# Performance work log

Measured on AMD Instinct MI355X. Metric: run time of the kernel, lower is better.

The kernel has to match this reference:

```python
import jax, jax.numpy as jnp
import numpy as np

H = 1024; NH = 16; HD = H // NH  # hidden, heads, head_dim

def setup_inputs() -> dict:
    key = jax.random.key(0)
    ks = jax.random.split(key, 9)
    s = 1.0 / np.sqrt(H)
    return {
        "hidden_states": jax.random.normal(ks[0], (2, 2048, H), jnp.float32),
        "Wq": jax.random.uniform(ks[1], (H, H), jnp.float32, -s, s),
        "bq": jnp.zeros((H,), jnp.float32),
        "Wk": jax.random.uniform(ks[2], (H, H), jnp.float32, -s, s),
        "bk": jnp.zeros((H,), jnp.float32),
        "Wv": jax.random.uniform(ks[3], (H, H), jnp.float32, -s, s),
        "bv": jnp.zeros((H,), jnp.float32),
        "Wo": jax.random.uniform(ks[4], (H, H), jnp.float32, -s, s),
        "bo": jnp.zeros((H,), jnp.float32),
    }

def reference(hidden_states, Wq, bq, Wk, bk, Wv, bv, Wo, bo):
    B, S, _ = hidden_states.shape
    def heads(x):  # [B,S,H] -> [B,NH,S,HD]
        return x.reshape(B, S, NH, HD).transpose(0, 2, 1, 3)
    q = heads(hidden_states @ Wq + bq)
    k = heads(hidden_states @ Wk + bk)
    v = heads(hidden_states @ Wv + bv)
    scores = jnp.einsum('bhqd,bhkd->bhqk', q, k) / jnp.sqrt(jnp.float32(HD))
    causal = jnp.where(jnp.tril(jnp.ones((S, S), bool)), 0.0, -jnp.inf)
    probs = jax.nn.softmax(scores + causal[None, None], axis=-1)
    ctx = jnp.einsum('bhqk,bhkd->bhqd', probs, v)
    ctx = ctx.transpose(0, 2, 1, 3).reshape(B, S, H)
    return ctx @ Wo + bo
```

## Files before the change

### kernel.cpp

```cpp
#include <hip/hip_runtime.h>
#include <hip/hip_bf16.h>

#define BB 2
#define SS 2048
#define HH 1024
#define NHH 16
#define HDD 64
#define MM (BB*SS)
#define QKV_N (3*HH)

typedef _Float16 f16x8 __attribute__((ext_vector_type(8)));
typedef _Float16 f16x4 __attribute__((ext_vector_type(4)));
typedef float f32x4 __attribute__((ext_vector_type(4)));

#define MFMA16(a,b,c)  __builtin_amdgcn_mfma_f32_16x16x32_f16((a),(b),(c),0,0,0)
#define MFMA16K16(a,b,c) __builtin_amdgcn_mfma_f32_16x16x16f16((a),(b),(c),0,0,0)

__device__ __forceinline__ void gl2lds16(const _Float16* g, _Float16* l) {
    __builtin_amdgcn_global_load_lds(
        (const __attribute__((address_space(1))) void*)g,
        (__attribute__((address_space(3))) void*)l, 16, 0, 0);
}

__device__ __forceinline__ float fexp2(float x) { return __builtin_amdgcn_exp2f(x); }

__global__ __launch_bounds__(256) void prep_kernel(
    const float* __restrict__ X,
    const float* __restrict__ W0, const float* __restrict__ W1,
    const float* __restrict__ W2, const float* __restrict__ W3,
    _Float16* __restrict__ Xh,
    _Float16* __restrict__ WqkvT, _Float16* __restrict__ WoT)
{
    __shared__ float t[64][65];
    int z = blockIdx.z;
    int tid = threadIdx.x;
    if (z == 4) {
        int base = (blockIdx.y * 16 + blockIdx.x) * 256 + tid;
        const float4* xin = (const float4*)X;
        f16x4* xout = (f16x4*)Xh;
#pragma unroll
        for (int i = 0; i < 16; ++i) {
            float4 v = xin[base + i * 65536];
            f16x4 hh = {(_Float16)v.x, (_Float16)v.y, (_Float16)v.z, (_Float16)v.w};
            xout[base + i * 65536] = hh;
        }
        return;
    }
    const float* src = (z == 0) ? W0 : (z == 1) ? W1 : (z == 2) ? W2 : W3;
    _Float16* dst = (z < 3) ? (WqkvT + (size_t)z * HH * HH) : WoT;
    int k0 = blockIdx.y * 64, n0 = blockIdx.x * 64;
#pragma unroll
    for (int p = 0; p < 4; ++p) {
        int row = p * 16 + (tid >> 4);
        int col4 = (tid & 15) * 4;
        float4 v = *(const float4*)&src[(size_t)(k0 + row) * HH + n0 + col4];
        t[row][col4 + 0] = v.x; t[row][col4 + 1] = v.y;
        t[row][col4 + 2] = v.z; t[row][col4 + 3] = v.w;
    }
    __syncthreads();
#pragma unroll
    for (int p = 0; p < 2; ++p) {
        int nc = p * 32 + (tid >> 3);
        int ch = tid & 7;
        f16x8 o;
#pragma unroll
        for (int j = 0; j < 8; ++j) o[j] = (_Float16)t[ch * 8 + j][nc];
        *(f16x8*)&dst[(size_t)(n0 + nc) * HH + k0 + ch * 8] = o;
    }
}

template<int MODE>
__global__ __launch_bounds__(256) void gemm128_kernel(
    const _Float16* __restrict__ A, const _Float16* __restrict__ Bt,
    const float* __restrict__ bias0, const float* __restrict__ bias1, const float* __restrict__ bias2,
    _Float16* __restrict__ Qh, _Float16* __restrict__ Kh, _Float16* __restrict__ Vt,
    float* __restrict__ Out)
{
    const int K = HH;
    const int NT = K / 32;
    __shared__ _Float16 smem[24576];

    int row0 = blockIdx.y * 128, n0 = blockIdx.x * 128;
    int tid = threadIdx.x;
    int w = tid >> 6, l = tid & 63, m16 = l & 15, quad = l >> 4;
    int wm = w >> 1, wn = w & 1;

    int srow = w * 32 + (l >> 2);
    int sch = (l & 3) ^ ((l >> 2) & 3) ^ ((l >> 4) & 3);
    const _Float16* aptr = A + (size_t)(row0 + srow) * K + sch * 8;
    const _Float16* bptr = Bt + (size_t)(n0 + srow) * K + sch * 8;

    int gsw = (m16 & 3) ^ ((m16 >> 2) & 3);
    int acol = (quad ^ gsw) * 8;

    f32x4 zero4 = {0.f, 0.f, 0.f, 0.f};
    f32x4 acc[4][4];
#pragma unroll
    for (int i = 0; i < 4; ++i)
#pragma unroll
        for (int j = 0; j < 4; ++j) acc[i][j] = zero4;

    auto stage = [&](int t, int s) {
        int k0 = t * 32;
        int ao = s * 4096 + (w * 32) * 32;
        int bo = 12288 + s * 4096 + (w * 32) * 32;
        gl2lds16(aptr + k0, smem + ao);
        gl2lds16(aptr + (size_t)16 * K + k0, smem + ao + 16 * 32);
        gl2lds16(bptr + k0, smem + bo);
        gl2lds16(bptr + (size_t)16 * K + k0, smem + bo + 16 * 32);
    };

    stage(0, 0);
    stage(1, 1);
    int cur = 0;
    for (int t = 0; t < NT; ++t) {
        if (t < NT - 1) asm volatile("s_waitcnt vmcnt(4)" ::: "memory");
        else            asm volatile("s_waitcnt vmcnt(0)" ::: "memory");
        asm volatile("s_barrier" ::: "memory");
        if (t + 2 < NT) {
            int nxt = cur + 2; if (nxt >= 3) nxt -= 3;
            stage(t + 2, nxt);
        }
        const _Float16* Asr = smem + cur * 4096;
        const _Float16* Bsr = smem + 12288 + cur * 4096;
        f16x8 af[4], bf[4];
#pragma unroll
        for (int i = 0; i < 4; ++i)
            af[i] = *(const f16x8*)&Asr[(wm * 64 + i * 16 + m16) * 32 + acol];
#pragma unroll
        for (int j = 0; j < 4; ++j)
            bf[j] = *(const f16x8*)&Bsr[(wn * 64 + j * 16 + m16) * 32 + acol];
#pragma unroll
        for (int i = 0; i < 4; ++i)
#pragma unroll
            for (int j = 0; j < 4; ++j)
                acc[i][j] = MFMA16(af[i], bf[j], acc[i][j]);
        cur = (cur == 2) ? 0 : cur + 1;
    }

    if (MODE == 1) {
#pragma unroll
        for (int j = 0; j < 4; ++j) {
            int n = n0 + wn * 64 + j * 16 + m16;
            float bi = bias0[n];
#pragma unroll
            for (int i = 0; i < 4; ++i)
#pragma unroll
                for (int r = 0; r < 4; ++r) {
                    int mg = row0 + wm * 64 + i * 16 + quad * 4 + r;
                    Out[(size_t)mg * HH + n] = acc[i][j][r] + bi;
                }
        }
        return;
    }

    int which = n0 >> 10;
    const float* bias = (which == 0) ? bias0 : (which == 1) ? bias1 : bias2;
    __syncthreads();
#pragma unroll
    for (int j = 0; j < 4; ++j) {
        int n_local = wn * 64 + j * 16 + m16;
        float bi = bias[(n0 + n_local) & 1023];
#pragma unroll
        for (int i = 0; i < 4; ++i)
#pragma unroll
            for (int r = 0; r < 4; ++r) {
                int m_local = wm * 64 + i * 16 + quad * 4 + r;
                float v = acc[i][j][r] + bi;
                if (which == 0) v *= 0.18033688011112042f;
                if (which == 2) smem[n_local * 132 + m_local] = (_Float16)v;
                else            smem[m_local * 132 + n_local] = (_Float16)v;
            }
    }
    __syncthreads();

    int b = row0 >> 11, s0 = row0 & 2047;
    if (which == 2) {
#pragma unroll
        for (int p = 0; p < 8; ++p) {
            int n_local = p * 16 + (tid >> 4);
            int schunk = tid & 15;
            f16x8 v = *(const f16x8*)&smem[n_local * 132 + schunk * 8];
            int nw = (n0 + n_local) & 1023;
            int hh = nw >> 6, d = nw & 63;
            *(f16x8*)&Vt[((size_t)(b * NHH + hh) * HDD + d) * SS + s0 + schunk * 8] = v;
        }
    } else {
        _Float16* dst = (which == 0) ? Qh : Kh;
        int hh0 = (n0 & 1023) >> 6;
#pragma unroll
        for (int p = 0; p < 8; ++p) {
            int m_local = p * 16 + (tid >> 4);
            int seg = tid & 15;
            f16x8 v = *(const f16x8*)&smem[m_local * 132 + seg * 8];
            int hh = hh0 + (seg >> 3), d = (seg & 7) * 8;
            *(f16x8*)&dst[((size_t)(b * NHH + hh) * SS + s0 + m_local) * HDD + d] = v;
        }
    }
}

__global__ __launch_bounds__(512, 4) void attn_kernel(
    const _Float16* __restrict__ Qh, const _Float16* __restrict__ Kh,
    const _Float16* __restrict__ Vt, _Float16* __restrict__ Ctx)
{
    __shared__ _Float16 KV[3 * 8192];

    int tid = threadIdx.x;
    int w = tid >> 6, l = tid & 63;
    int m16 = l & 15, quad = l >> 4;
    int b = blockIdx.z, h = blockIdx.y;
    int tA = blockIdx.x, tB = 31 - tA;
    int half = w >> 2, wq = w & 3;
    int myT = half ? tB : tA;

    const _Float16* Q = Qh + (size_t)(b * NHH + h) * SS * HDD;
    const _Float16* K = Kh + (size_t)(b * NHH + h) * SS * HDD;
    const _Float16* V = Vt + (size_t)(b * NHH + h) * HDD * SS;

    int q = myT * 64 + wq * 16 + m16;
    f16x8 aq0 = *(const f16x8*)(Q + (size_t)q * HDD + quad * 8);
    f16x8 aq1 = *(const f16x8*)(Q + (size_t)q * HDD + 32 + quad * 8);

    int srow = w * 8 + (l >> 3);
    int sch = (l & 7) ^ (l >> 3);
    const _Float16* kg = K + (size_t)srow * HDD + sch * 8;
    const _Float16* vg = V + (size_t)srow * SS + sch * 8;

    auto stage = [&](int t, int s) {
        int kt = t * 64;
        _Float16* kb = &KV[s * 8192];
        _Float16* vb = &KV[s * 8192 + 4096];
        gl2lds16(kg + (size_t)kt * HDD, kb + (w * 8) * 64);
        gl2lds16(vg + kt, vb + (w * 8) * 64);
    };

    int swz = m16 & 7;
    int cka = (quad ^ swz) * 8;
    int ckb = ((quad + 4) ^ swz) * 8;
    int vco[4];
#pragma unroll
    for (int s = 0; s < 4; ++s)
        vco[s] = (((s * 2 + (quad >> 1)) ^ swz) * 8) + (quad & 1) * 4;

    f32x4 zero4 = {0.f, 0.f, 0.f, 0.f};
    const f16x4 ones4 = {(_Float16)1.f, (_Float16)1.f, (_Float16)1.f, (_Float16)1.f};
    f32x4 o[4];
#pragma unroll
    for (int c = 0; c < 4; ++c) o[c] = zero4;
    f32x4 lacc = zero4;

    stage(0, 0);
    stage(1, 1);
    int cur = 0;
    for (int t = 0; t <= tB; ++t) {
        int kt = t * 64;
        if (t < tB) asm volatile("s_waitcnt vmcnt(2)" ::: "memory");
        else        asm volatile("s_waitcnt vmcnt(0)" ::: "memory");
        asm volatile("s_barrier" ::: "memory");
        if (t + 2 <= tB) {
            int nxt = cur + 2; if (nxt >= 3) nxt -= 3;
            stage(t + 2, nxt);
        }

        if (t <= myT) {
            const _Float16* kb = &KV[cur * 8192];
            const _Float16* vb = &KV[cur * 8192 + 4096];
            f16x8 bk[4][2];
#pragma unroll
            for (int s = 0; s < 4; ++s) {
                const _Float16* kr = kb + (s * 16 + m16) * 64;
                bk[s][0] = *(const f16x8*)(kr + cka);
                bk[s][1] = *(const f16x8*)(kr + ckb);
            }
            f16x4 av[4][4];
#pragma unroll
            for (int c = 0; c < 4; ++c) {
                const _Float16* vr = vb + (c * 16 + m16) * 64;
#pragma unroll
                for (int s = 0; s < 4; ++s)
                    av[c][s] = *(const f16x4*)(vr + vco[s]);
            }

            f32x4 st[4];
#pragma unroll
            for (int s = 0; s < 4; ++s) {
                st[s] = MFMA16(bk[s][0], aq0, zero4);
                st[s] = MFMA16(bk[s][1], aq1, st[s]);
            }
            f16x4 pt[4];
            if (t == myT) {
#pragma unroll
                for (int s = 0; s < 4; ++s)
#pragma unroll
                    for (int r = 0; r < 4; ++r) {
                        float p = fexp2(st[s][r]);
                        int key = kt + s * 16 + quad * 4 + r;
                        if (key > q) p = 0.f;
                        pt[s][r] = (_Float16)p;
                    }
            } else {
#pragma unroll
                for (int s = 0; s < 4; ++s)
#pragma unroll
                    for (int r = 0; r < 4; ++r)
                        pt[s][r] = (_Float16)fexp2(st[s][r]);
            }
#pragma unroll
            for (int s = 0; s < 4; ++s)
                lacc = MFMA16K16(ones4, pt[s], lacc);
#pragma unroll
            for (int c = 0; c < 4; ++c)
#pragma unroll
                for (int s = 0; s < 4; ++s)
                    o[c] = MFMA16K16(av[c][s], pt[s], o[c]);
        }

        cur = (cur == 2) ? 0 : cur + 1;
    }

    float inv = 1.0f / lacc[0];
    size_t rowoff = ((size_t)(b * SS) + q) * HH + h * HDD;
#pragma unroll
    for (int c = 0; c < 4; ++c) {
        f16x4 ov;
#pragma unroll
        for (int r = 0; r < 4; ++r) ov[r] = (_Float16)(o[c][r] * inv);
        *(f16x4*)&Ctx[rowoff + c * 16 + quad * 4] = ov;
    }
}

extern "C" void kernel_launch(void* const* d_in, const int* in_sizes, int n_in,
                              void* d_out, int out_size, void* d_ws, size_t ws_size,
                              hipStream_t stream) {
    const float* hs = (const float*)d_in[0];
    const float* Wq = (const float*)d_in[1];
    const float* bq = (const float*)d_in[2];
    const float* Wk = (const float*)d_in[3];
    const float* bk = (const float*)d_in[4];
    const float* Wv = (const float*)d_in[5];
    const float* bv = (const float*)d_in[6];
    const float* Wo = (const float*)d_in[7];
    const float* bo = (const float*)d_in[8];
    float* out = (float*)d_out;

    size_t off = 0;
    auto alloc = [&](size_t bytes) {
        void* p = (char*)d_ws + off;
        off += (bytes + 255) & ~(size_t)255;
        return p;
    };
    _Float16* Xh    = (_Float16*)alloc((size_t)MM * HH * 2);
    _Float16* WqkvT = (_Float16*)alloc((size_t)3 * HH * HH * 2);
    _Float16* WoT   = (_Float16*)alloc((size_t)HH * HH * 2);
    _Float16* Qh    = (_Float16*)alloc((size_t)BB * NHH * SS * HDD * 2);
    _Float16* Kh    = (_Float16*)alloc((size_t)BB * NHH * SS * HDD * 2);
    _Float16* Vt    = (_Float16*)alloc((size_t)BB * NHH * SS * HDD * 2);
    _Float16* Ctx   = (_Float16*)alloc((size_t)MM * HH * 2);

    prep_kernel<<<dim3(16, 16, 5), 256, 0, stream>>>(
        hs, Wq, Wk, Wv, Wo, Xh, WqkvT, WoT);
    gemm128_kernel<0><<<dim3(QKV_N / 128, MM / 128), 256, 0, stream>>>(
        Xh, WqkvT, bq, bk, bv, Qh, Kh, Vt, nullptr);
    attn_kernel<<<dim3(16, NHH, BB), 512, 0, stream>>>(Qh, Kh, Vt, Ctx);
    gemm128_kernel<1><<<dim3(HH / 128, MM / 128), 256, 0, stream>>>(
        Ctx, WoT, bo, bo, bo, nullptr, nullptr, nullptr, out);
}
```

Before: 181.2 us.

## Use 256x256-tile 8-wave GEMM with XCD-aware block swizzle for QKV projection

Adds a new QKV projection GEMM that uses 256x256 output tiles with 512 threads and double-buffered direct global-to-LDS loads. Prefetch of the next K-slice is interleaved with the MFMA groups, and s_setprio raises priority around the MFMAs. Workgroup IDs are remapped in a swizzle across groups of 8, apparently to match the MI355X's XCDs and improve L2 reuse. The aim is more data reuse per loaded tile and fewer global reads, at the cost of a smaller grid (192 blocks), heavier register pressure, and an epilogue split into four passes through LDS.

```diff
diff --git a/kernel.cpp b/kernel.cpp
--- a/kernel.cpp
+++ b/kernel.cpp
@@ -69,6 +69,149 @@
     }
 }
 
+__global__ __launch_bounds__(512, 2) void gemm256_kernel(
+    const _Float16* __restrict__ A, const _Float16* __restrict__ Bt,
+    const float* __restrict__ bias0, const float* __restrict__ bias1, const float* __restrict__ bias2,
+    _Float16* __restrict__ Qh, _Float16* __restrict__ Kh, _Float16* __restrict__ Vt)
+{
+    const int K = HH;
+    const int NT = K / 32;
+    __shared__ _Float16 smem[32768];
+
+    int nwgx = gridDim.x;
+    int bid = blockIdx.y * nwgx + blockIdx.x;
+    int nwg = nwgx * gridDim.y;
+    int swzb = (bid & 7) * (nwg >> 3) + (bid >> 3);
+    int bx = swzb % nwgx, by = swzb / nwgx;
+    int row0 = by * 256, n0 = bx * 256;
+
+    int tid = threadIdx.x;
+    int w = tid >> 6, l = tid & 63, m16 = l & 15, quad = l >> 4;
+    int wm = w >> 2, wn = w & 3;
+
+    int sch = (l & 3) ^ ((l >> 2) & 3) ^ ((l >> 4) & 3);
+    const _Float16* aptr = A + (size_t)(row0 + w * 16 + (l >> 2)) * K + sch * 8;
+    const _Float16* bptr = Bt + (size_t)(n0 + w * 16 + (l >> 2)) * K + sch * 8;
+
+    int gsw = (m16 & 3) ^ ((m16 >> 2) & 3);
+    int acol = (quad ^ gsw) * 8;
+
+    f32x4 zero4 = {0.f, 0.f, 0.f, 0.f};
+    f32x4 acc[8][4];
+#pragma unroll
+    for (int i = 0; i < 8; ++i)
+#pragma unroll
+        for (int j = 0; j < 4; ++j) acc[i][j] = zero4;
+
+    auto stageA = [&](int t, int j) {
+        int s = (t & 1) * 16384;
+        gl2lds16(aptr + (size_t)j * 128 * K + t * 32, smem + s + (j * 128 + w * 16) * 32);
+    };
+    auto stageB = [&](int t, int j) {
+        int s = (t & 1) * 16384;
+        gl2lds16(bptr + (size_t)j * 128 * K + t * 32, smem + s + 8192 + (j * 128 + w * 16) * 32);
+    };
+
+    stageA(0, 0); stageA(0, 1); stageB(0, 0); stageB(0, 1);
+
+    for (int t = 0; t < NT; ++t) {
+        const _Float16* As = smem + (t & 1) * 16384;
+        const _Float16* Bs = As + 8192;
+        bool pf = (t + 1 < NT);
+
+        if (pf) { stageA(t + 1, 0); asm volatile("s_waitcnt vmcnt(1)" ::: "memory"); }
+        else    {                   asm volatile("s_waitcnt vmcnt(0)" ::: "memory"); }
+        asm volatile("s_barrier" ::: "memory");
+        f16x8 bf[4];
+#pragma unroll
+        for (int j = 0; j < 4; ++j)
+            bf[j] = *(const f16x8*)&Bs[(wn * 64 + j * 16 + m16) * 32 + acol];
+        {
+            f16x8 a0 = *(const f16x8*)&As[(wm * 128 + m16) * 32 + acol];
+            f16x8 a1 = *(const f16x8*)&As[(wm * 128 + 16 + m16) * 32 + acol];
+            __builtin_amdgcn_s_setprio(1);
+#pragma unroll
+            for (int j = 0; j < 4; ++j) acc[0][j] = MFMA16(a0, bf[j], acc[0][j]);
+#pragma unroll
+            for (int j = 0; j < 4; ++j) acc[1][j] = MFMA16(a1, bf[j], acc[1][j]);
+            __builtin_amdgcn_s_setprio(0);
+        }
+
+#pragma unroll
+        for (int p = 1; p < 4; ++p) {
+            f16x8 a0 = *(const f16x8*)&As[(wm * 128 + (2 * p) * 16 + m16) * 32 + acol];
+            f16x8 a1 = *(const f16x8*)&As[(wm * 128 + (2 * p + 1) * 16 + m16) * 32 + acol];
+            if (pf) {
+                if (p == 1) stageA(t + 1, 1);
+                else if (p == 2) stageB(t + 1, 0);
+                else stageB(t + 1, 1);
+            }
+            asm volatile("s_barrier" ::: "memory");
+            __builtin_amdgcn_s_setprio(1);
+#pragma unroll
+            for (int j = 0; j < 4; ++j) acc[2 * p][j] = MFMA16(a0, bf[j], acc[2 * p][j]);
+#pragma unroll
+            for (int j = 0; j < 4; ++j) acc[2 * p + 1][j] = MFMA16(a1, bf[j], acc[2 * p + 1][j]);
+            __builtin_amdgcn_s_setprio(0);
+        }
+        asm volatile("s_barrier" ::: "memory");
+    }
+
+    int which = n0 >> 10;
+    const float* bias = (which == 0) ? bias0 : (which == 1) ? bias1 : bias2;
+    int b = row0 >> 11, s0 = row0 & 2047;
+    _Float16* es = smem;
+
+#pragma unroll
+    for (int rh = 0; rh < 2; ++rh)
+#pragma unroll
+    for (int ch = 0; ch < 2; ++ch) {
+        __syncthreads();
+        if (wm == rh && (wn >> 1) == ch) {
+#pragma unroll
+            for (int j = 0; j < 4; ++j) {
+                int n_local = (wn & 1) * 64 + j * 16 + m16;
+                float bi = bias[(n0 + ch * 128 + n_local) & 1023];
+#pragma unroll
+                for (int i = 0; i < 8; ++i)
+#pragma unroll
+                    for (int r = 0; r < 4; ++r) {
+                        int m_local = i * 16 + quad * 4 + r;
+                        float v = acc[i][j][r] + bi;
+                        if (which == 0) v *= 0.18033688011112042f;
+                        if (which == 2) es[n_local * 132 + m_local] = (_Float16)v;
+                        else            es[m_local * 132 + n_local] = (_Float16)v;
+                    }
+            }
+        }
+        __syncthreads();
+        int hn0 = n0 + ch * 128;
+        int hs0 = s0 + rh * 128;
+        if (which == 2) {
+#pragma unroll
+            for (int p = 0; p < 4; ++p) {
+                int n_local = p * 32 + (tid >> 4);
+                int schunk = tid & 15;
+                f16x8 v = *(const f16x8*)&es[n_local * 132 + schunk * 8];
+                int nw = (hn0 + n_local) & 1023;
+                int hh = nw >> 6, d = nw & 63;
+                *(f16x8*)&Vt[((size_t)(b * NHH + hh) * HDD + d) * SS + hs0 + schunk * 8] = v;
+            }
+        } else {
+            _Float16* dst = (which == 0) ? Qh : Kh;
+            int hh0 = (hn0 & 1023) >> 6;
+#pragma unroll
+            for (int p = 0; p < 4; ++p) {
+                int m_local = p * 32 + (tid >> 4);
+                int seg = tid & 15;
+                f16x8 v = *(const f16x8*)&es[m_local * 132 + seg * 8];
+                int hh = hh0 + (seg >> 3), d = (seg & 7) * 8;
+                *(f16x8*)&dst[((size_t)(b * NHH + hh) * SS + hs0 + m_local) * HDD + d] = v;
+            }
+        }
+    }
+}
+
 template<int MODE>
 __global__ __launch_bounds__(256) void gemm128_kernel(
     const _Float16* __restrict__ A, const _Float16* __restrict__ Bt,
@@ -359,8 +502,8 @@
 
     prep_kernel<<<dim3(16, 16, 5), 256, 0, stream>>>(
         hs, Wq, Wk, Wv, Wo, Xh, WqkvT, WoT);
-    gemm128_kernel<0><<<dim3(QKV_N / 128, MM / 128), 256, 0, stream>>>(
-        Xh, WqkvT, bq, bk, bv, Qh, Kh, Vt, nullptr);
+    gemm256_kernel<<<dim3(QKV_N / 256, MM / 256), 512, 0, stream>>>(
+        Xh, WqkvT, bq, bk, bv, Qh, Kh, Vt);
     attn_kernel<<<dim3(16, NHH, BB), 512, 0, stream>>>(Qh, Kh, Vt, Ctx);
     gemm128_kernel<1><<<dim3(HH / 128, MM / 128), 256, 0, stream>>>(
         Ctx, WoT, bo, bo, bo, nullptr, nullptr, nullptr, out);
```

Result: slower. 199.1 us (+9.8%).

## Split paired causal tiles into one 256-thread block per query tile

Applied to the files above, without the earlier changes.

The attention kernel previously paired query tile t with tile 31-t inside a 512-thread block so every block did balanced work, with a triple-buffered K/V pipeline two tiles deep. It now launches one 256-thread block per 64-row query tile, longest tiles first, and uses a double-buffered pipeline that prefetches one tile ahead, with two barriers per iteration. This drops idle half-block iterations and the shared K/V loads they wasted, and lowers LDS use per block to allow more resident blocks. In exchange it relies on the hardware scheduler for load balance across uneven causal tiles and has a shallower prefetch.

```diff
diff --git a/kernel.cpp b/kernel.cpp
--- a/kernel.cpp
+++ b/kernel.cpp
@@ -199,39 +199,39 @@
     }
 }
 
-__global__ __launch_bounds__(512, 4) void attn_kernel(
+__global__ __launch_bounds__(256, 5) void attn_kernel(
     const _Float16* __restrict__ Qh, const _Float16* __restrict__ Kh,
     const _Float16* __restrict__ Vt, _Float16* __restrict__ Ctx)
 {
-    __shared__ _Float16 KV[3 * 8192];
+    __shared__ _Float16 KV[2 * 8192];
 
     int tid = threadIdx.x;
     int w = tid >> 6, l = tid & 63;
     int m16 = l & 15, quad = l >> 4;
     int b = blockIdx.z, h = blockIdx.y;
-    int tA = blockIdx.x, tB = 31 - tA;
-    int half = w >> 2, wq = w & 3;
-    int myT = half ? tB : tA;
+    int tq = 31 - blockIdx.x;
 
     const _Float16* Q = Qh + (size_t)(b * NHH + h) * SS * HDD;
     const _Float16* K = Kh + (size_t)(b * NHH + h) * SS * HDD;
     const _Float16* V = Vt + (size_t)(b * NHH + h) * HDD * SS;
 
-    int q = myT * 64 + wq * 16 + m16;
+    int q = tq * 64 + w * 16 + m16;
     f16x8 aq0 = *(const f16x8*)(Q + (size_t)q * HDD + quad * 8);
     f16x8 aq1 = *(const f16x8*)(Q + (size_t)q * HDD + 32 + quad * 8);
 
-    int srow = w * 8 + (l >> 3);
+    int srow = w * 16 + (l >> 3);
     int sch = (l & 7) ^ (l >> 3);
     const _Float16* kg = K + (size_t)srow * HDD + sch * 8;
     const _Float16* vg = V + (size_t)srow * SS + sch * 8;
 
-    auto stage = [&](int t, int s) {
+    auto stage = [&](int t) {
         int kt = t * 64;
-        _Float16* kb = &KV[s * 8192];
-        _Float16* vb = &KV[s * 8192 + 4096];
-        gl2lds16(kg + (size_t)kt * HDD, kb + (w * 8) * 64);
-        gl2lds16(vg + kt, vb + (w * 8) * 64);
+        _Float16* kb = &KV[(t & 1) * 8192];
+        _Float16* vb = &KV[(t & 1) * 8192 + 4096];
+        gl2lds16(kg + (size_t)kt * HDD, kb + (w * 16) * 64);
+        gl2lds16(kg + (size_t)(kt + 8) * HDD, kb + (w * 16 + 8) * 64);
+        gl2lds16(vg + kt, vb + (w * 16) * 64);
+        gl2lds16(vg + (size_t)8 * SS + kt, vb + (w * 16 + 8) * 64);
     };
 
     int swz = m16 & 7;
@@ -249,73 +249,68 @@
     for (int c = 0; c < 4; ++c) o[c] = zero4;
     f32x4 lacc = zero4;
 
-    stage(0, 0);
-    stage(1, 1);
-    int cur = 0;
-    for (int t = 0; t <= tB; ++t) {
+    stage(0);
+    for (int t = 0; t <= tq; ++t) {
         int kt = t * 64;
-        if (t < tB) asm volatile("s_waitcnt vmcnt(2)" ::: "memory");
-        else        asm volatile("s_waitcnt vmcnt(0)" ::: "memory");
         asm volatile("s_barrier" ::: "memory");
-        if (t + 2 <= tB) {
-            int nxt = cur + 2; if (nxt >= 3) nxt -= 3;
-            stage(t + 2, nxt);
-        }
-
-        if (t <= myT) {
-            const _Float16* kb = &KV[cur * 8192];
-            const _Float16* vb = &KV[cur * 8192 + 4096];
-            f16x8 bk[4][2];
-#pragma unroll
-            for (int s = 0; s < 4; ++s) {
-                const _Float16* kr = kb + (s * 16 + m16) * 64;
-                bk[s][0] = *(const f16x8*)(kr + cka);
-                bk[s][1] = *(const f16x8*)(kr + ckb);
-            }
-            f16x4 av[4][4];
-#pragma unroll
-            for (int c = 0; c < 4; ++c) {
-                const _Float16* vr = vb + (c * 16 + m16) * 64;
-#pragma unroll
-                for (int s = 0; s < 4; ++s)
-                    av[c][s] = *(const f16x4*)(vr + vco[s]);
-            }
-
-            f32x4 st[4];
-#pragma unroll
-            for (int s = 0; s < 4; ++s) {
-                st[s] = MFMA16(bk[s][0], aq0, zero4);
-                st[s] = MFMA16(bk[s][1], aq1, st[s]);
-            }
-            f16x4 pt[4];
-            if (t == myT) {
-#pragma unroll
-                for (int s = 0; s < 4; ++s)
-#pragma unroll
-                    for (int r = 0; r < 4; ++r) {
-                        float p = fexp2(st[s][r]);
-                        int key = kt + s * 16 + quad * 4 + r;
-                        if (key > q) p = 0.f;
-                        pt[s][r] = (_Float16)p;
-                    }
-            } else {
-#pragma unroll
-                for (int s = 0; s < 4; ++s)
-#pragma unroll
-                    for (int r = 0; r < 4; ++r)
-                        pt[s][r] = (_Float16)fexp2(st[s][r]);
-            }
+        if (t + 1 <= tq) {
+            stage(t + 1);
+            asm volatile("s_waitcnt vmcnt(4)" ::: "memory");
+        } else {
+            asm volatile("s_waitcnt vmcnt(0)" ::: "memory");
+        }
+        asm volatile("s_barrier" ::: "memory");
+
+        const _Float16* kb = &KV[(t & 1) * 8192];
+        const _Float16* vb = &KV[(t & 1) * 8192 + 4096];
+        f16x8 bk[4][2];
+#pragma unroll
+        for (int s = 0; s < 4; ++s) {
+            const _Float16* kr = kb + (s * 16 + m16) * 64;
+            bk[s][0] = *(const f16x8*)(kr + cka);
+            bk[s][1] = *(const f16x8*)(kr + ckb);
+        }
+        f16x4 av[4][4];
+#pragma unroll
+        for (int c = 0; c < 4; ++c) {
+            const _Float16* vr = vb + (c * 16 + m16) * 64;
 #pragma unroll
             for (int s = 0; s < 4; ++s)
-                lacc = MFMA16K16(ones4, pt[s], lacc);
-#pragma unroll
-            for (int c = 0; c < 4; ++c)
-#pragma unroll
-                for (int s = 0; s < 4; ++s)
-                    o[c] = MFMA16K16(av[c][s], pt[s], o[c]);
-        }
-
-        cur = (cur == 2) ? 0 : cur + 1;
+                av[c][s] = *(const f16x4*)(vr + vco[s]);
+        }
+
+        f32x4 st[4];
+#pragma unroll
+        for (int s = 0; s < 4; ++s) {
+            st[s] = MFMA16(bk[s][0], aq0, zero4);
+            st[s] = MFMA16(bk[s][1], aq1, st[s]);
+        }
+        f16x4 pt[4];
+        if (t == tq) {
+#pragma unroll
+            for (int s = 0; s < 4; ++s)
+#pragma unroll
+                for (int r = 0; r < 4; ++r) {
+                    float p = fexp2(st[s][r]);
+                    int key = kt + s * 16 + quad * 4 + r;
+                    if (key > q) p = 0.f;
+                    pt[s][r] = (_Float16)p;
+                }
+        } else {
+#pragma unroll
+            for (int s = 0; s < 4; ++s)
+#pragma unroll
+                for (int r = 0; r < 4; ++r)
+                    pt[s][r] = (_Float16)fexp2(st[s][r]);
+        }
+#pragma unroll
+        for (int s = 0; s < 4; ++s)
+            lacc = MFMA16K16(ones4, pt[s], lacc);
+#pragma unroll
+        for (int c = 0; c < 4; ++c)
+#pragma unroll
+            for (int s = 0; s < 4; ++s)
+                o[c] = MFMA16K16(av[c][s], pt[s], o[c]);
     }
 
     float inv = 1.0f / lacc[0];
@@ -361,7 +356,7 @@
         hs, Wq, Wk, Wv, Wo, Xh, WqkvT, WoT);
     gemm128_kernel<0><<<dim3(QKV_N / 128, MM / 128), 256, 0, stream>>>(
         Xh, WqkvT, bq, bk, bv, Qh, Kh, Vt, nullptr);
-    attn_kernel<<<dim3(16, NHH, BB), 512, 0, stream>>>(Qh, Kh, Vt, Ctx);
+    attn_kernel<<<dim3(32, NHH, BB), 256, 0, stream>>>(Qh, Kh, Vt, Ctx);
     gemm128_kernel<1><<<dim3(HH / 128, MM / 128), 256, 0, stream>>>(
         Ctx, WoT, bo, bo, bo, nullptr, nullptr, nullptr, out);
 }
```

After: 204.3 us. +12.7%, slower.
